# Kernel optimization log

Measured on AMD Instinct MI355X. Metric: run time of the kernel, lower is better.

Reference implementation:

```python
import jax, jax.numpy as jnp
import numpy as np

B, S, D = 4, 2048, 1024
H = 16
DH = D // H  # 64
THETA = 10000.0


def setup_inputs() -> dict:
    key = jax.random.key(0)
    ks = jax.random.split(key, 7)
    scale = 1.0 / np.sqrt(D)
    return {
        "Q": jax.random.normal(ks[0], (B, S, D), dtype=jnp.float32),
        "K": jax.random.normal(ks[1], (B, S, D), dtype=jnp.float32),
        "V": jax.random.normal(ks[2], (B, S, D), dtype=jnp.float32),
        "Wq": jax.random.normal(ks[3], (D, D), dtype=jnp.float32) * scale,
        "Wk": jax.random.normal(ks[4], (D, D), dtype=jnp.float32) * scale,
        "Wv": jax.random.normal(ks[5], (D, D), dtype=jnp.float32) * scale,
        "Wo": jax.random.normal(ks[6], (D, D), dtype=jnp.float32) * scale,
    }


def _rope_tables(seq_len, d_head, theta, dtype):
    inv_freq = 1.0 / theta ** (jnp.arange(0, d_head, 2, dtype=jnp.float32) / d_head)
    ang = jnp.arange(seq_len, dtype=jnp.float32)[:, None] * inv_freq[None, :]  # [S, DH/2]
    return jnp.sin(ang).astype(dtype), jnp.cos(ang).astype(dtype)


def _apply_rope(x, sin, cos):
    # x: [B, H, S, DH]; sin/cos: [S, DH/2] broadcast over B,H
    x1 = x[..., 0::2]
    x2 = x[..., 1::2]
    x1r = x1 * cos - x2 * sin
    x2r = x1 * sin + x2 * cos
    return jnp.stack([x1r, x2r], axis=-1).reshape(x.shape)


def reference(Q, K, V, Wq, Wk, Wv, Wo):
    seq_len = Q.shape[-2]
    q = Q @ Wq.T
    k = K @ Wk.T
    v = V @ Wv.T

    def split(x):  # [B, S, D] -> [B, H, S, DH]
        return x.reshape(x.shape[0], seq_len, H, DH).transpose(0, 2, 1, 3)

    qh, kh, vh = split(q), split(k), split(v)

    sin, cos = _rope_tables(seq_len, DH, THETA, qh.dtype)
    qh = _apply_rope(qh, sin, cos)
    kh = _apply_rope(kh, sin, cos)

    # attention in fp32 (matches original cast)
    qf = qh.astype(jnp.float32)
    kf = kh.astype(jnp.float32)
    vf = vh.astype(jnp.float32)
    scale = 1.0 / np.sqrt(DH)
    scores = jnp.einsum('bhqd,bhkd->bhqk', qf, kf) * scale
    causal = jnp.tril(jnp.ones((seq_len, seq_len), dtype=bool))
    scores = jnp.where(causal, scores, -jnp.inf)
    attn = jax.nn.softmax(scores, axis=-1)
    out_h = jnp.einsum('bhqk,bhkd->bhqd', attn, vf).astype(Q.dtype)

    out = out_h.transpose(0, 2, 1, 3).reshape(Q.shape[0], seq_len, D)
    return out @ Wo.T
```

## Files before the change

kernel.cpp:

```cpp
#include <hip/hip_runtime.h>
#include <hip/hip_bf16.h>
#include <cmath>

#define B_ 4
#define S_ 2048
#define D_ 1024
#define H_ 16
#define DH_ 64

typedef __bf16 bf16_t;
typedef __bf16 bf16x8 __attribute__((ext_vector_type(8)));
typedef __bf16 bf16x4 __attribute__((ext_vector_type(4)));
typedef float f32x4 __attribute__((ext_vector_type(4)));

static __device__ __forceinline__ f32x4 mfma16(bf16x8 a, bf16x8 b, f32x4 c) {
    return __builtin_amdgcn_mfma_f32_16x16x32_bf16(a, b, c, 0, 0, 0);
}

static __device__ __forceinline__ float fast_exp2(float x) {
#if __has_builtin(__builtin_amdgcn_exp2f)
    return __builtin_amdgcn_exp2f(x);
#else
    float r; asm("v_exp_f32 %0, %1" : "=v"(r) : "v"(x)); return r;
#endif
}

static __device__ __forceinline__ void glds16(const void* g, void* l) {
    __builtin_amdgcn_global_load_lds(
        (const __attribute__((address_space(1))) unsigned int*)g,
        (__attribute__((address_space(3))) unsigned int*)l, 16, 0, 0);
}

__global__ __launch_bounds__(256)
void prep_kernel(const float* __restrict__ Wq, const float* __restrict__ Wk,
                 const float* __restrict__ Wv, const float* __restrict__ Wo,
                 bf16_t* __restrict__ Wb, float2* __restrict__ tab)
{
    int bid = blockIdx.x;
    if (bid < 256) {
        int idx = bid * 256 + threadIdx.x;
        int s = idx >> 5, i = idx & 31;
        float inv = powf(10000.f, -(2.f * i) / 64.f);
        float ang = (float)s * inv;
        tab[idx] = make_float2(sinf(ang), cosf(ang));
    } else {
        int i = (bid - 256) * 256 + threadIdx.x;
        int t = i >> 17, j = i & 131071;
        const float* src = (t == 0) ? Wq : (t == 1) ? Wk : (t == 2) ? Wv : Wo;
        const float4* s = (const float4*)(src + (size_t)j * 8);
        float4 a = s[0], b = s[1];
        bf16x8 v = { (__bf16)a.x, (__bf16)a.y, (__bf16)a.z, (__bf16)a.w,
                     (__bf16)b.x, (__bf16)b.y, (__bf16)b.z, (__bf16)b.w };
        *(bf16x8*)(Wb + (size_t)i * 8) = v;
    }
}

template<int EPI>
__global__ __launch_bounds__(256)
void proj_kernel(const float* __restrict__ X, const bf16_t* __restrict__ W,
                 bf16_t* __restrict__ dst, const float2* __restrict__ tab)
{
    __shared__ bf16x8 lA[128 * 8];
    __shared__ bf16x8 lB[128 * 8];
    const int tid = threadIdx.x;
    const int gm0 = blockIdx.x * 128;
    const int gn0 = blockIdx.y * 128;
    const int wid = tid >> 6, lane = tid & 63;
    const int lr = lane & 15, lh = lane >> 4;
    const int wm = (wid >> 1) * 64, wn = (wid & 1) * 64;

    int arow[4], aslot[4];
    const float* abase[4];
    #pragma unroll
    for (int i = 0; i < 4; ++i) {
        int slot = i * 256 + tid;
        int row = slot >> 3, s = slot & 7, c = s ^ (row & 7);
        arow[i] = row; aslot[i] = s;
        abase[i] = X + (size_t)(gm0 + row) * D_ + c * 8;
    }
    float4 av0[4], av1[4];
    #pragma unroll
    for (int i = 0; i < 4; ++i) {
        av0[i] = *(const float4*)(abase[i]);
        av1[i] = *(const float4*)(abase[i] + 4);
    }

    f32x4 acc[4][4] = {};

    #pragma unroll 1
    for (int kt = 0; kt < D_ / 64; ++kt) {
        __syncthreads();
        #pragma unroll
        for (int i = 0; i < 4; ++i) {
            int base = wid * 64 + i * 256;
            int slot = base + lane;
            int row = slot >> 3, s = slot & 7, c = s ^ (row & 7);
            glds16(W + (size_t)(gn0 + row) * D_ + kt * 64 + c * 8, &lB[base]);
        }
        #pragma unroll
        for (int i = 0; i < 4; ++i) {
            lA[arow[i] * 8 + aslot[i]] = bf16x8{
                (__bf16)av0[i].x, (__bf16)av0[i].y, (__bf16)av0[i].z, (__bf16)av0[i].w,
                (__bf16)av1[i].x, (__bf16)av1[i].y, (__bf16)av1[i].z, (__bf16)av1[i].w };
        }
        __syncthreads();
        if (kt + 1 < D_ / 64) {
            #pragma unroll
            for (int i = 0; i < 4; ++i) {
                av0[i] = *(const float4*)(abase[i] + (kt + 1) * 64);
                av1[i] = *(const float4*)(abase[i] + (kt + 1) * 64 + 4);
            }
        }
        #pragma unroll
        for (int ks = 0; ks < 2; ++ks) {
            bf16x8 af[4], bfr[4];
            int kh8 = ks * 4 + lh;
            #pragma unroll
            for (int mi = 0; mi < 4; ++mi) { int r = wm + mi * 16 + lr; af[mi]  = lA[r * 8 + (kh8 ^ (r & 7))]; }
            #pragma unroll
            for (int ni = 0; ni < 4; ++ni) { int r = wn + ni * 16 + lr; bfr[ni] = lB[r * 8 + (kh8 ^ (r & 7))]; }
            #pragma unroll
            for (int mi = 0; mi < 4; ++mi)
                #pragma unroll
                for (int ni = 0; ni < 4; ++ni)
                    acc[mi][ni] = mfma16(af[mi], bfr[ni], acc[mi][ni]);
        }
    }

    #pragma unroll
    for (int mi = 0; mi < 4; ++mi) {
        #pragma unroll
        for (int j = 0; j < 4; ++j) {
            int m = gm0 + wm + mi * 16 + lh * 4 + j;
            int b = m >> 11, s = m & (S_ - 1);
            #pragma unroll
            for (int ni = 0; ni < 4; ++ni) {
                int n = gn0 + wn + ni * 16 + lr;
                int h = n >> 6, dh = n & 63;
                float x = acc[mi][ni][j];
                if (EPI == 0) {
                    float p = __shfl_xor(x, 1);
                    float2 sc = tab[s * 32 + (dh >> 1)];
                    float r = (dh & 1) ? (p * sc.x + x * sc.y)
                                       : (x * sc.y - p * sc.x);
                    dst[(((size_t)b * H_ + h) * S_ + s) * DH_ + dh] = (bf16_t)r;
                } else {
                    dst[(((size_t)b * H_ + h) * DH_ + dh) * S_ + s] = (bf16_t)x;
                }
            }
        }
    }
}

__global__ __launch_bounds__(256, 4)
void attn_kernel(const bf16_t* __restrict__ qh, const bf16_t* __restrict__ kh,
                 const bf16_t* __restrict__ vT, bf16_t* __restrict__ O)
{
    __shared__ bf16x8 lK[2][64 * 8];
    __shared__ bf16x8 lV[2][64 * 8];
    __shared__ bf16x8 lP8[4][128];
    const int tid = threadIdx.x, wid = tid >> 6, lane = tid & 63;
    const int lr = lane & 15, lh = lane >> 4;
    const int bh = blockIdx.x & 63;
    const int t  = 31 - (blockIdx.x >> 6);
    const bf16_t* Qp = qh + (size_t)bh * S_ * DH_;
    const bf16_t* Kp = kh + (size_t)bh * S_ * DH_;
    const bf16_t* Vp = vT + (size_t)bh * DH_ * S_;
    char* lP = (char*)lP8[wid];
    const int b = bh >> 4, h = bh & 15;
    const float QSCALE = 0.125f * 1.44269504f;
    const int wq = t * 64 + wid * 16;

    const bf16_t* kga[2]; const bf16_t* vga[2]; int sbase[2];
    #pragma unroll
    for (int i = 0; i < 2; ++i) {
        int base = i * 256 + (wid << 6);
        int slot = base + lane;
        int row = slot >> 3, s = slot & 7, c = s ^ (row & 7);
        sbase[i] = base;
        kga[i] = Kp + (size_t)row * DH_ + c * 8;
        vga[i] = Vp + (size_t)row * S_ + c * 8;
    }

    bf16x8 qf[2];
    #pragma unroll
    for (int ks = 0; ks < 2; ++ks) {
        bf16x8 q8 = *(const bf16x8*)(Qp + (size_t)(wq + lr) * DH_ + ks * 32 + lh * 8);
        #pragma unroll
        for (int e = 0; e < 8; ++e) q8[e] = (__bf16)((float)q8[e] * QSCALE);
        qf[ks] = q8;
    }

    f32x4 accO[4] = {};
    float mrun = -1e30f, lrun = 0.f;
    const int nkt = t + 1;

    #pragma unroll
    for (int i = 0; i < 2; ++i) {
        glds16(kga[i], &lK[0][sbase[i]]);
        glds16(vga[i], &lV[0][sbase[i]]);
    }
    __syncthreads();
    int cur = 0;

    #pragma unroll 1
    for (int kt = 0; kt < nkt; ++kt) {
        if (kt + 1 < nkt) {
            #pragma unroll
            for (int i = 0; i < 2; ++i) {
                glds16(kga[i] + (size_t)(kt + 1) * 64 * DH_, &lK[cur ^ 1][sbase[i]]);
                glds16(vga[i] + (size_t)(kt + 1) * 64,       &lV[cur ^ 1][sbase[i]]);
            }
        }

        f32x4 sc[4] = {};
        __builtin_amdgcn_s_setprio(1);
        #pragma unroll
        for (int ks = 0; ks < 2; ++ks) {
            int kh8 = ks * 4 + lh;
            #pragma unroll
            for (int kvi = 0; kvi < 4; ++kvi) {
                int r = kvi * 16 + lr;
                bf16x8 kf = lK[cur][r * 8 + (kh8 ^ (r & 7))];
                sc[kvi] = mfma16(kf, qf[ks], sc[kvi]);
            }
        }
        __builtin_amdgcn_s_setprio(0);

        const int kvb = kt * 64 + 4 * lh;
        const int qg = wq + lr;
        float pv[16];
        if (kt == t) {
            #pragma unroll
            for (int kvi = 0; kvi < 4; ++kvi)
                #pragma unroll
                for (int j = 0; j < 4; ++j) {
                    float x = sc[kvi][j];
                    if ((kvb + kvi * 16 + j) > qg) x = -1e30f;
                    pv[kvi * 4 + j] = x;
                }
        } else {
            #pragma unroll
            for (int kvi = 0; kvi < 4; ++kvi)
                #pragma unroll
                for (int j = 0; j < 4; ++j) pv[kvi * 4 + j] = sc[kvi][j];
        }

        float t0 = fmaxf(fmaxf(pv[0],  pv[1]),  pv[2]);
        float t1 = fmaxf(fmaxf(pv[3],  pv[4]),  pv[5]);
        float t2 = fmaxf(fmaxf(pv[6],  pv[7]),  pv[8]);
        float t3 = fmaxf(fmaxf(pv[9],  pv[10]), pv[11]);
        float t4 = fmaxf(fmaxf(pv[12], pv[13]), pv[14]);
        float u0 = fmaxf(fmaxf(t0, t1), t2);
        float u1 = fmaxf(fmaxf(t3, t4), pv[15]);
        float mxp = fmaxf(u0, u1);

        float mnew = mrun;
        bool skip = __all(mxp <= mrun + 8.0f);
        if (!skip) {
            float mx = fmaxf(mxp, __shfl_xor(mxp, 16));
            mx = fmaxf(mx, __shfl_xor(mx, 32));
            mnew = fmaxf(mrun, mx);
            float rs = fast_exp2(mrun - mnew);
            mrun = mnew;
            lrun *= rs;
            #pragma unroll
            for (int j = 0; j < 4; ++j) {
                float rj = __shfl(rs, 4 * lh + j);
                #pragma unroll
                for (int ni = 0; ni < 4; ++ni) accO[ni][j] *= rj;
            }
        }
        #pragma unroll
        for (int i = 0; i < 16; ++i) pv[i] = fast_exp2(pv[i] - mnew);
        float s8[8], s4v[4];
        #pragma unroll
        for (int i = 0; i < 8; ++i) s8[i] = pv[i] + pv[i + 8];
        #pragma unroll
        for (int i = 0; i < 4; ++i) s4v[i] = s8[i] + s8[i + 4];
        lrun += (s4v[0] + s4v[1]) + (s4v[2] + s4v[3]);

        #pragma unroll
        for (int kvi = 0; kvi < 4; ++kvi) {
            bf16x4 hv = { (__bf16)pv[kvi * 4 + 0], (__bf16)pv[kvi * 4 + 1],
                          (__bf16)pv[kvi * 4 + 2], (__bf16)pv[kvi * 4 + 3] };
            int slot = 2 * kvi + (lh >> 1);
            *(bf16x4*)(lP + lr * 128 + ((slot ^ (lr & 7)) * 16) + (lh & 1) * 8) = hv;
        }

        __builtin_amdgcn_s_setprio(1);
        #pragma unroll
        for (int ks = 0; ks < 2; ++ks) {
            int kh8 = ks * 4 + lh;
            int slot = 4 * ks + lh;
            bf16x8 pf = *(const bf16x8*)(lP + lr * 128 + ((slot ^ (lr & 7)) * 16));
            #pragma unroll
            for (int ni = 0; ni < 4; ++ni) {
                int r = ni * 16 + lr;
                bf16x8 vf = lV[cur][r * 8 + (kh8 ^ (r & 7))];
                accO[ni] = mfma16(pf, vf, accO[ni]);
            }
        }
        __builtin_amdgcn_s_setprio(0);

        __syncthreads();
        cur ^= 1;
    }

    lrun += __shfl_xor(lrun, 16);
    lrun += __shfl_xor(lrun, 32);

    #pragma unroll
    for (int j = 0; j < 4; ++j) {
        int s = wq + 4 * lh + j;
        float inv = 1.f / __shfl(lrun, 4 * lh + j);
        #pragma unroll
        for (int ni = 0; ni < 4; ++ni) {
            int dh = ni * 16 + lr;
            O[((size_t)(b * S_ + s)) * D_ + h * DH_ + dh] = (bf16_t)(accO[ni][j] * inv);
        }
    }
}

__global__ __launch_bounds__(256)
void out_kernel(const bf16_t* __restrict__ A, const bf16_t* __restrict__ W,
                float* __restrict__ out)
{
    __shared__ bf16x8 lA[128 * 8];
    __shared__ bf16x8 lB[128 * 8];
    const int tid = threadIdx.x;
    const int gm0 = blockIdx.x * 128;
    const int gn0 = blockIdx.y * 128;
    const int wid = tid >> 6, lane = tid & 63;
    const int lr = lane & 15, lh = lane >> 4;
    const int wm = (wid >> 1) * 64, wn = (wid & 1) * 64;

    f32x4 acc[4][4] = {};

    for (int kt = 0; kt < D_ / 64; ++kt) {
        const int k0 = kt * 64;
        __syncthreads();
        #pragma unroll
        for (int i = 0; i < 4; ++i) {
            int base = wid * 64 + i * 256;
            int slot = base + lane;
            int row = slot >> 3, s = slot & 7, c = s ^ (row & 7);
            glds16(A + (size_t)(gm0 + row) * D_ + k0 + c * 8, &lA[base]);
            glds16(W + (size_t)(gn0 + row) * D_ + k0 + c * 8, &lB[base]);
        }
        __syncthreads();
        #pragma unroll
        for (int ks = 0; ks < 2; ++ks) {
            bf16x8 af[4], bfr[4];
            int kh = ks * 4 + lh;
            #pragma unroll
            for (int mi = 0; mi < 4; ++mi) { int r = wm + mi * 16 + lr; af[mi]  = lA[r * 8 + (kh ^ (r & 7))]; }
            #pragma unroll
            for (int ni = 0; ni < 4; ++ni) { int r = wn + ni * 16 + lr; bfr[ni] = lB[r * 8 + (kh ^ (r & 7))]; }
            #pragma unroll
            for (int mi = 0; mi < 4; ++mi)
                #pragma unroll
                for (int ni = 0; ni < 4; ++ni)
                    acc[mi][ni] = mfma16(af[mi], bfr[ni], acc[mi][ni]);
        }
    }

    #pragma unroll
    for (int mi = 0; mi < 4; ++mi)
        #pragma unroll
        for (int j = 0; j < 4; ++j) {
            int m = gm0 + wm + mi * 16 + lh * 4 + j;
            #pragma unroll
            for (int ni = 0; ni < 4; ++ni) {
                int n = gn0 + wn + ni * 16 + lr;
                out[(size_t)m * D_ + n] = acc[mi][ni][j];
            }
        }
}

extern "C" void kernel_launch(void* const* d_in, const int* in_sizes, int n_in,
                              void* d_out, int out_size, void* d_ws, size_t ws_size,
                              hipStream_t stream)
{
    const float* Q  = (const float*)d_in[0];
    const float* K  = (const float*)d_in[1];
    const float* V  = (const float*)d_in[2];
    const float* Wq = (const float*)d_in[3];
    const float* Wk = (const float*)d_in[4];
    const float* Wv = (const float*)d_in[5];
    const float* Wo = (const float*)d_in[6];
    float* out = (float*)d_out;

    char* ws = (char*)d_ws;
    const size_t MB = 1024 * 1024;
    bf16_t* qh  = (bf16_t*)(ws);
    bf16_t* khb = (bf16_t*)(ws + 16 * MB);
    bf16_t* vT  = (bf16_t*)(ws + 32 * MB);
    bf16_t* Ob  = (bf16_t*)(ws + 48 * MB);
    bf16_t* Wb  = (bf16_t*)(ws + 64 * MB);
    float2* tab = (float2*)(ws + 72 * MB);

    prep_kernel<<<2304, 256, 0, stream>>>(Wq, Wk, Wv, Wo, Wb, tab);

    dim3 g(64, 8);
    proj_kernel<0><<<g, 256, 0, stream>>>(Q, Wb + 0 * 1048576, qh, tab);
    proj_kernel<0><<<g, 256, 0, stream>>>(K, Wb + 1 * 1048576, khb, tab);
    proj_kernel<1><<<g, 256, 0, stream>>>(V, Wb + 2 * 1048576, vT, tab);

    attn_kernel<<<2048, 256, 0, stream>>>(qh, khb, vT, Ob);

    out_kernel<<<dim3(64, 8), 256, 0, stream>>>(Ob, Wb + 3 * 1048576, out);
}
```

Measured before the change: 181.6 us.

## Pair causal query tiles per block and widen per-wave query rows

The attention kernel now launches 512 blocks. Each block handles two 128-row query tiles (p and 15-p) in sequence, which balances causal work across blocks. Each wave processes 32 query rows instead of 16, so every K/V fragment read from LDS feeds twice as many MFMAs. The double-buffered async K/V prefetch is replaced by a single buffer with two barriers per tile, which exposes load latency, and the larger per-wave register and P-buffer state may reduce occupancy.

```diff
diff --git a/kernel.cpp b/kernel.cpp
--- a/kernel.cpp
+++ b/kernel.cpp
@@ -156,20 +156,19 @@
 void attn_kernel(const bf16_t* __restrict__ qh, const bf16_t* __restrict__ kh,
                  const bf16_t* __restrict__ vT, bf16_t* __restrict__ O)
 {
-    __shared__ bf16x8 lK[2][64 * 8];
-    __shared__ bf16x8 lV[2][64 * 8];
-    __shared__ bf16x8 lP8[4][128];
+    __shared__ bf16x8 lK[64 * 8];
+    __shared__ bf16x8 lV[64 * 8];
+    __shared__ bf16x8 lP4[4][256];
     const int tid = threadIdx.x, wid = tid >> 6, lane = tid & 63;
     const int lr = lane & 15, lh = lane >> 4;
     const int bh = blockIdx.x & 63;
-    const int t  = 31 - (blockIdx.x >> 6);
+    const int p  = blockIdx.x >> 6;
     const bf16_t* Qp = qh + (size_t)bh * S_ * DH_;
     const bf16_t* Kp = kh + (size_t)bh * S_ * DH_;
     const bf16_t* Vp = vT + (size_t)bh * DH_ * S_;
-    char* lP = (char*)lP8[wid];
+    char* lP = (char*)lP4[wid];
     const int b = bh >> 4, h = bh & 15;
     const float QSCALE = 0.125f * 1.44269504f;
-    const int wq = t * 64 + wid * 16;
 
     const bf16_t* kga[2]; const bf16_t* vga[2]; int sbase[2];
     #pragma unroll
@@ -182,142 +181,154 @@
         vga[i] = Vp + (size_t)row * S_ + c * 8;
     }
 
-    bf16x8 qf[2];
-    #pragma unroll
-    for (int ks = 0; ks < 2; ++ks) {
-        bf16x8 q8 = *(const bf16x8*)(Qp + (size_t)(wq + lr) * DH_ + ks * 32 + lh * 8);
-        #pragma unroll
-        for (int e = 0; e < 8; ++e) q8[e] = (__bf16)((float)q8[e] * QSCALE);
-        qf[ks] = q8;
-    }
-
-    f32x4 accO[4] = {};
-    float mrun = -1e30f, lrun = 0.f;
-    const int nkt = t + 1;
-
-    #pragma unroll
-    for (int i = 0; i < 2; ++i) {
-        glds16(kga[i], &lK[0][sbase[i]]);
-        glds16(vga[i], &lV[0][sbase[i]]);
-    }
-    __syncthreads();
-    int cur = 0;
-
     #pragma unroll 1
-    for (int kt = 0; kt < nkt; ++kt) {
-        if (kt + 1 < nkt) {
+    for (int ph = 0; ph < 2; ++ph) {
+        const int q0 = (ph == 0 ? (15 - p) : p) * 128;
+        const int wq = q0 + wid * 32;
+
+        bf16x8 qf[2][2];
+        #pragma unroll
+        for (int qi = 0; qi < 2; ++qi)
+            #pragma unroll
+            for (int ks = 0; ks < 2; ++ks) {
+                bf16x8 q8 = *(const bf16x8*)(Qp + (size_t)(wq + qi * 16 + lr) * DH_ + ks * 32 + lh * 8);
+                #pragma unroll
+                for (int e = 0; e < 8; ++e) q8[e] = (__bf16)((float)q8[e] * QSCALE);
+                qf[qi][ks] = q8;
+            }
+
+        f32x4 accO[2][4] = {};
+        float mrun[2] = { -1e30f, -1e30f };
+        float lrun[2] = { 0.f, 0.f };
+        const int nkt = q0 / 64 + 2;
+
+        #pragma unroll 1
+        for (int kt = 0; kt < nkt; ++kt) {
+            __syncthreads();
             #pragma unroll
             for (int i = 0; i < 2; ++i) {
-                glds16(kga[i] + (size_t)(kt + 1) * 64 * DH_, &lK[cur ^ 1][sbase[i]]);
-                glds16(vga[i] + (size_t)(kt + 1) * 64,       &lV[cur ^ 1][sbase[i]]);
-            }
-        }
-
-        f32x4 sc[4] = {};
-        __builtin_amdgcn_s_setprio(1);
-        #pragma unroll
-        for (int ks = 0; ks < 2; ++ks) {
-            int kh8 = ks * 4 + lh;
-            #pragma unroll
-            for (int kvi = 0; kvi < 4; ++kvi) {
-                int r = kvi * 16 + lr;
-                bf16x8 kf = lK[cur][r * 8 + (kh8 ^ (r & 7))];
-                sc[kvi] = mfma16(kf, qf[ks], sc[kvi]);
-            }
-        }
-        __builtin_amdgcn_s_setprio(0);
-
-        const int kvb = kt * 64 + 4 * lh;
-        const int qg = wq + lr;
-        float pv[16];
-        if (kt == t) {
-            #pragma unroll
-            for (int kvi = 0; kvi < 4; ++kvi)
-                #pragma unroll
-                for (int j = 0; j < 4; ++j) {
-                    float x = sc[kvi][j];
-                    if ((kvb + kvi * 16 + j) > qg) x = -1e30f;
-                    pv[kvi * 4 + j] = x;
-                }
-        } else {
-            #pragma unroll
-            for (int kvi = 0; kvi < 4; ++kvi)
-                #pragma unroll
-                for (int j = 0; j < 4; ++j) pv[kvi * 4 + j] = sc[kvi][j];
-        }
-
-        float t0 = fmaxf(fmaxf(pv[0],  pv[1]),  pv[2]);
-        float t1 = fmaxf(fmaxf(pv[3],  pv[4]),  pv[5]);
-        float t2 = fmaxf(fmaxf(pv[6],  pv[7]),  pv[8]);
-        float t3 = fmaxf(fmaxf(pv[9],  pv[10]), pv[11]);
-        float t4 = fmaxf(fmaxf(pv[12], pv[13]), pv[14]);
-        float u0 = fmaxf(fmaxf(t0, t1), t2);
-        float u1 = fmaxf(fmaxf(t3, t4), pv[15]);
-        float mxp = fmaxf(u0, u1);
-
-        float mnew = mrun;
-        bool skip = __all(mxp <= mrun + 8.0f);
-        if (!skip) {
-            float mx = fmaxf(mxp, __shfl_xor(mxp, 16));
-            mx = fmaxf(mx, __shfl_xor(mx, 32));
-            mnew = fmaxf(mrun, mx);
-            float rs = fast_exp2(mrun - mnew);
-            mrun = mnew;
-            lrun *= rs;
+                glds16(kga[i] + (size_t)kt * 64 * DH_, &lK[sbase[i]]);
+                glds16(vga[i] + (size_t)kt * 64,       &lV[sbase[i]]);
+            }
+            __syncthreads();
+
+            if (kt * 64 > wq + 31) continue;
+
+            f32x4 sc[4][2] = {};
+            __builtin_amdgcn_s_setprio(1);
+            #pragma unroll
+            for (int ks = 0; ks < 2; ++ks) {
+                int kh8 = ks * 4 + lh;
+                #pragma unroll
+                for (int kvi = 0; kvi < 4; ++kvi) {
+                    int r = kvi * 16 + lr;
+                    bf16x8 kf = lK[r * 8 + (kh8 ^ (r & 7))];
+                    #pragma unroll
+                    for (int qi = 0; qi < 2; ++qi)
+                        sc[kvi][qi] = mfma16(kf, qf[qi][ks], sc[kvi][qi]);
+                }
+            }
+            __builtin_amdgcn_s_setprio(0);
+
+            const bool needm = (kt * 64 + 63 > wq);
+            const int kvb = kt * 64 + 4 * lh;
+            #pragma unroll
+            for (int qi = 0; qi < 2; ++qi) {
+                const int qg = wq + qi * 16 + lr;
+                float pv[16];
+                #pragma unroll
+                for (int kvi = 0; kvi < 4; ++kvi)
+                    #pragma unroll
+                    for (int j = 0; j < 4; ++j) {
+                        float x = sc[kvi][qi][j];
+                        if (needm && (kvb + kvi * 16 + j) > qg) x = -1e30f;
+                        pv[kvi * 4 + j] = x;
+                    }
+
+                float t0 = fmaxf(fmaxf(pv[0],  pv[1]),  pv[2]);
+                float t1 = fmaxf(fmaxf(pv[3],  pv[4]),  pv[5]);
+                float t2 = fmaxf(fmaxf(pv[6],  pv[7]),  pv[8]);
+                float t3 = fmaxf(fmaxf(pv[9],  pv[10]), pv[11]);
+                float t4 = fmaxf(fmaxf(pv[12], pv[13]), pv[14]);
+                float u0 = fmaxf(fmaxf(t0, t1), t2);
+                float u1 = fmaxf(fmaxf(t3, t4), pv[15]);
+                float mxp = fmaxf(u0, u1);
+
+                float mnew = mrun[qi];
+                bool skip = __all(mxp <= mnew + 8.0f);
+                if (!skip) {
+                    float mx = fmaxf(mxp, __shfl_xor(mxp, 16));
+                    mx = fmaxf(mx, __shfl_xor(mx, 32));
+                    mnew = fmaxf(mrun[qi], mx);
+                    float rs = fast_exp2(mrun[qi] - mnew);
+                    mrun[qi] = mnew;
+                    lrun[qi] *= rs;
+                    #pragma unroll
+                    for (int j = 0; j < 4; ++j) {
+                        float rj = __shfl(rs, 4 * lh + j);
+                        #pragma unroll
+                        for (int ni = 0; ni < 4; ++ni) accO[qi][ni][j] *= rj;
+                    }
+                }
+                #pragma unroll
+                for (int i = 0; i < 16; ++i) pv[i] = fast_exp2(pv[i] - mnew);
+                float s8[8], s4v[4];
+                #pragma unroll
+                for (int i = 0; i < 8; ++i) s8[i] = pv[i] + pv[i + 8];
+                #pragma unroll
+                for (int i = 0; i < 4; ++i) s4v[i] = s8[i] + s8[i + 4];
+                lrun[qi] += (s4v[0] + s4v[1]) + (s4v[2] + s4v[3]);
+
+                const int qhat = qi * 16 + lr;
+                #pragma unroll
+                for (int kvi = 0; kvi < 4; ++kvi) {
+                    bf16x4 hv = { (__bf16)pv[kvi * 4 + 0], (__bf16)pv[kvi * 4 + 1],
+                                  (__bf16)pv[kvi * 4 + 2], (__bf16)pv[kvi * 4 + 3] };
+                    int slot = 2 * kvi + (lh >> 1);
+                    *(bf16x4*)(lP + qhat * 128 + ((slot ^ (qhat & 7)) * 16) + (lh & 1) * 8) = hv;
+                }
+            }
+
+            __builtin_amdgcn_s_setprio(1);
+            #pragma unroll
+            for (int ks = 0; ks < 2; ++ks) {
+                int kh8 = ks * 4 + lh;
+                int slot = 4 * ks + lh;
+                bf16x8 pf[2], vf[4];
+                #pragma unroll
+                for (int mi = 0; mi < 2; ++mi) {
+                    int row = mi * 16 + lr;
+                    pf[mi] = *(const bf16x8*)(lP + row * 128 + ((slot ^ (row & 7)) * 16));
+                }
+                #pragma unroll
+                for (int ni = 0; ni < 4; ++ni) {
+                    int r = ni * 16 + lr;
+                    vf[ni] = lV[r * 8 + (kh8 ^ (r & 7))];
+                }
+                #pragma unroll
+                for (int mi = 0; mi < 2; ++mi)
+                    #pragma unroll
+                    for (int ni = 0; ni < 4; ++ni)
+                        accO[mi][ni] = mfma16(pf[mi], vf[ni], accO[mi][ni]);
+            }
+            __builtin_amdgcn_s_setprio(0);
+        }
+
+        #pragma unroll
+        for (int mi = 0; mi < 2; ++mi) {
+            float lsum = lrun[mi];
+            lsum += __shfl_xor(lsum, 16);
+            lsum += __shfl_xor(lsum, 32);
             #pragma unroll
             for (int j = 0; j < 4; ++j) {
-                float rj = __shfl(rs, 4 * lh + j);
-                #pragma unroll
-                for (int ni = 0; ni < 4; ++ni) accO[ni][j] *= rj;
-            }
-        }
-        #pragma unroll
-        for (int i = 0; i < 16; ++i) pv[i] = fast_exp2(pv[i] - mnew);
-        float s8[8], s4v[4];
-        #pragma unroll
-        for (int i = 0; i < 8; ++i) s8[i] = pv[i] + pv[i + 8];
-        #pragma unroll
-        for (int i = 0; i < 4; ++i) s4v[i] = s8[i] + s8[i + 4];
-        lrun += (s4v[0] + s4v[1]) + (s4v[2] + s4v[3]);
-
-        #pragma unroll
-        for (int kvi = 0; kvi < 4; ++kvi) {
-            bf16x4 hv = { (__bf16)pv[kvi * 4 + 0], (__bf16)pv[kvi * 4 + 1],
-                          (__bf16)pv[kvi * 4 + 2], (__bf16)pv[kvi * 4 + 3] };
-            int slot = 2 * kvi + (lh >> 1);
-            *(bf16x4*)(lP + lr * 128 + ((slot ^ (lr & 7)) * 16) + (lh & 1) * 8) = hv;
-        }
-
-        __builtin_amdgcn_s_setprio(1);
-        #pragma unroll
-        for (int ks = 0; ks < 2; ++ks) {
-            int kh8 = ks * 4 + lh;
-            int slot = 4 * ks + lh;
-            bf16x8 pf = *(const bf16x8*)(lP + lr * 128 + ((slot ^ (lr & 7)) * 16));
-            #pragma unroll
-            for (int ni = 0; ni < 4; ++ni) {
-                int r = ni * 16 + lr;
-                bf16x8 vf = lV[cur][r * 8 + (kh8 ^ (r & 7))];
-                accO[ni] = mfma16(pf, vf, accO[ni]);
-            }
-        }
-        __builtin_amdgcn_s_setprio(0);
-
-        __syncthreads();
-        cur ^= 1;
-    }
-
-    lrun += __shfl_xor(lrun, 16);
-    lrun += __shfl_xor(lrun, 32);
-
-    #pragma unroll
-    for (int j = 0; j < 4; ++j) {
-        int s = wq + 4 * lh + j;
-        float inv = 1.f / __shfl(lrun, 4 * lh + j);
-        #pragma unroll
-        for (int ni = 0; ni < 4; ++ni) {
-            int dh = ni * 16 + lr;
-            O[((size_t)(b * S_ + s)) * D_ + h * DH_ + dh] = (bf16_t)(accO[ni][j] * inv);
+                int s = wq + mi * 16 + 4 * lh + j;
+                float inv = 1.f / __shfl(lsum, 4 * lh + j);
+                #pragma unroll
+                for (int ni = 0; ni < 4; ++ni) {
+                    int dh = ni * 16 + lr;
+                    O[((size_t)(b * S_ + s)) * D_ + h * DH_ + dh] = (bf16_t)(accO[mi][ni][j] * inv);
+                }
+            }
         }
     }
 }
@@ -407,7 +418,7 @@
     proj_kernel<0><<<g, 256, 0, stream>>>(K, Wb + 1 * 1048576, khb, tab);
     proj_kernel<1><<<g, 256, 0, stream>>>(V, Wb + 2 * 1048576, vT, tab);
 
-    attn_kernel<<<2048, 256, 0, stream>>>(qh, khb, vT, Ob);
+    attn_kernel<<<512, 256, 0, stream>>>(qh, khb, vT, Ob);
 
     out_kernel<<<dim3(64, 8), 256, 0, stream>>>(Ob, Wb + 3 * 1048576, out);
 }
```

Result: slower. 232.2 us (+27.8%).
